# Kernel tuning notes

Hardware: AMD Instinct MI355X
Metric: run time of the kernel (lower is better)

The kernel has to match this reference:

```python
import jax, jax.numpy as jnp
import numpy as np
from jax import lax

B, T, H, C = 1024, 128, 256, 10


def setup_inputs() -> dict:
    key = jax.random.key(0)
    ks = jax.random.split(key, 16)
    inp = {
        "x": jax.random.normal(ks[0], (B, T), dtype=jnp.float32),
        # torch.randn-initialized input weights (input_dim=1)
        "w_gx": jax.random.normal(ks[1], (1, H), dtype=jnp.float32),
        "w_ix": jax.random.normal(ks[2], (1, H), dtype=jnp.float32),
        "w_fx": jax.random.normal(ks[3], (1, H), dtype=jnp.float32),
        "w_ox": jax.random.normal(ks[4], (1, H), dtype=jnp.float32),
        # torch.rand-initialized recurrent weights
        "w_gh": jax.random.uniform(ks[5], (H, H), dtype=jnp.float32),
        "w_ih": jax.random.uniform(ks[6], (H, H), dtype=jnp.float32),
        "w_fh": jax.random.uniform(ks[7], (H, H), dtype=jnp.float32),
        "w_oh": jax.random.uniform(ks[8], (H, H), dtype=jnp.float32),
        "b_g": jax.random.uniform(ks[9], (H,), dtype=jnp.float32),
        "b_i": jax.random.uniform(ks[10], (H,), dtype=jnp.float32),
        "b_f": jax.random.uniform(ks[11], (H,), dtype=jnp.float32),
        "b_o": jax.random.uniform(ks[12], (H,), dtype=jnp.float32),
        "w_ph": jax.random.normal(ks[13], (H, C), dtype=jnp.float32),
        "b_p": jax.random.uniform(ks[14], (C,), dtype=jnp.float32),
    }
    return inp


def reference(x, w_gx, w_ix, w_fx, w_ox, w_gh, w_ih, w_fh, w_oh,
              b_g, b_i, b_f, b_o, w_ph, b_p):
    # Fuse the 4 gate projections into one GEMM per step (same math, order: g,i,f,o)
    Wx = jnp.concatenate([w_gx, w_ix, w_fx, w_ox], axis=1)   # (1, 4H)
    Wh = jnp.concatenate([w_gh, w_ih, w_fh, w_oh], axis=1)   # (H, 4H)
    b = jnp.concatenate([b_g, b_i, b_f, b_o])                 # (4H,)
    h0 = jnp.zeros((x.shape[0], w_gh.shape[0]), dtype=x.dtype)
    c0 = jnp.zeros_like(h0)

    def step(carry, xt):
        h, c = carry
        # xt: (B,) scalar input per example -> (B,1) @ (1,4H)
        z = xt[:, None] @ Wx + h @ Wh + b                     # (B, 4H)
        g, i, f, o = jnp.split(z, 4, axis=1)
        g = jnp.tanh(g)
        i = jax.nn.sigmoid(i)
        f = jax.nn.sigmoid(f)
        o = jax.nn.sigmoid(o)
        c = g * i + c * f
        h = jnp.tanh(c) * o
        return (h, c), None

    (h, _), _ = lax.scan(step, (h0, c0), x.T)                  # scan over time (T, B)
    return h @ w_ph + b_p                                      # (B, num_classes)
```

## Files before the change

kernel.cpp:

```cpp
#include <hip/hip_runtime.h>


#define TSTEPS  128
#define HDIM    256
#define NCLS    10
#define BB      4
#define NBLOCKS 256
#define NTHR    512

#define XSTR    132
#define HSTR    320
#define PSTR    260

typedef char  i8x16 __attribute__((ext_vector_type(16)));
typedef int   i32x4 __attribute__((ext_vector_type(4)));

#define L2E     1.4426950408889634f
#define MGC     (-2.0f * L2E)
#define SMG     (-2.0f * L2E / 16129.0f)
#define SMS     (-1.0f * L2E / 16129.0f)

static __device__ __forceinline__ float rcpf(float x) { return __builtin_amdgcn_rcpf(x); }
static __device__ __forceinline__ float exp2f_fast(float x) { return __builtin_amdgcn_exp2f(x); }

#define MFMA_I8(ACC, A, B) \
    asm("v_mfma_i32_16x16x64_i8 %0, %1, %2, %0" : "+v"(ACC) : "v"(A), "a"(B))

__global__ __launch_bounds__(64)
void pack_w(const float* __restrict__ wg, const float* __restrict__ wi,
            const float* __restrict__ wf, const float* __restrict__ wo,
            signed char* __restrict__ wq8)
{
    const int b = blockIdx.x;
    const int q = b >> 8;
    const int u = b & 255;
    const float* wp = (q == 0) ? wg : (q == 1) ? wi : (q == 2) ? wf : wo;
    const int t  = threadIdx.x;
    const int k0 = t * 4;
    unsigned int pk = 0;
#pragma unroll
    for (int i = 0; i < 4; ++i) {
        const float v = wp[(k0 + i) * HDIM + u];
        int qv = __float2int_rn(v * 127.0f);
        qv = (qv > 127) ? 127 : ((qv < -127) ? -127 : qv);
        pk |= ((unsigned int)qv & 255u) << (8 * i);
    }
    *(unsigned int*)(wq8 + ((size_t)(q * 256 + u) * 256 + k0)) = pk;
}

__global__ __launch_bounds__(NTHR, 2)
void lstm_full(const float* __restrict__ x,
               const float* __restrict__ w_gx, const float* __restrict__ w_ix,
               const float* __restrict__ w_fx, const float* __restrict__ w_ox,
               const float* __restrict__ b_g,  const float* __restrict__ b_i,
               const float* __restrict__ b_f,  const float* __restrict__ b_o,
               const float* __restrict__ w_ph, const float* __restrict__ b_p,
               const signed char* __restrict__ wq8,
               float* __restrict__ out)
{
    const int g    = blockIdx.x;
    const int tid  = threadIdx.x;
    const int w    = tid >> 6;
    const int lane = tid & 63;
    const int l16  = lane & 15;
    const int lq   = lane >> 4;

    __shared__ float        x_lds[BB * XSTR];
    __shared__ signed char  h_q[2][BB * HSTR];
    __shared__ float        proj[BB * PSTR];

    {
        const float* xs = x + (size_t)g * BB * TSTEPS;
        for (int i = tid; i < BB * TSTEPS; i += NTHR)
            x_lds[(i >> 7) * XSTR + (i & 127)] = xs[i];
    }

    i32x4 wa[4][2][4];
#pragma unroll
    for (int q = 0; q < 4; ++q)
#pragma unroll
        for (int ut = 0; ut < 2; ++ut) {
            const int u = w * 32 + ut * 16 + l16;
#pragma unroll
            for (int kk = 0; kk < 4; ++kk) {
                const signed char* p = wq8 + ((size_t)(q * 256 + u) * 256)
                                           + kk * 64 + lq * 16;
                i32x4 v = __builtin_bit_cast(i32x4, *(const i8x16*)p);
                asm volatile("" : "+a"(v));
                wa[q][ut][kk] = v;
            }
        }

    const float* const wxp[4] = {w_gx, w_ix, w_fx, w_ox};
    const float* const bbp[4] = {b_g, b_i, b_f, b_o};
    float wxm[4][2], bm[4][2];
#pragma unroll
    for (int q = 0; q < 4; ++q)
#pragma unroll
        for (int ut = 0; ut < 2; ++ut) {
            const int u = w * 32 + ut * 16 + l16;
            const float m = (q == 0) ? MGC : (-L2E);
            wxm[q][ut] = wxp[q][u] * m;
            bm[q][ut]  = bbp[q][u] * m;
        }

    float c[2] = {0.f, 0.f};
    const bool s0 = (lq & 1) != 0;
    const bool s1 = (lq & 2) != 0;

    __syncthreads();

    for (int t = 0; t < TSTEPS; ++t) {
        i32x4 ah[4];
        if (t > 0) {
            const signed char* hs = &h_q[t & 1][(l16 & 3) * HSTR];
#pragma unroll
            for (int kk = 0; kk < 4; ++kk)
                ah[kk] = *(const i32x4*)(hs + kk * 64 + lq * 16);
        }

        i32x4 a0[4] = {{0,0,0,0},{0,0,0,0},{0,0,0,0},{0,0,0,0}};
        i32x4 a1[4] = {{0,0,0,0},{0,0,0,0},{0,0,0,0},{0,0,0,0}};
        if (t > 0) {
#pragma unroll
            for (int kk = 0; kk < 4; ++kk)
#pragma unroll
                for (int q = 0; q < 4; ++q)
                    MFMA_I8(a0[q], ah[kk], wa[q][0][kk]);
#pragma unroll
            for (int kk = 0; kk < 4; ++kk)
#pragma unroll
                for (int q = 0; q < 4; ++q)
                    MFMA_I8(a1[q], ah[kk], wa[q][1][kk]);
        }

        const float xv = x_lds[lq * XSTR + t];
        signed char* hd = &h_q[(t + 1) & 1][0];
#pragma unroll
        for (int ut = 0; ut < 2; ++ut) {
            float zs[4];
#pragma unroll
            for (int q = 0; q < 4; ++q) {
                const i32x4 v = ut ? a1[q] : a0[q];
                const int lo = s0 ? v[1] : v[0];
                const int hi = s0 ? v[3] : v[2];
                const int av = s1 ? hi : lo;
                const float sm = (q == 0) ? SMG : SMS;
                zs[q] = __builtin_fmaf((float)av, sm,
                        __builtin_fmaf(xv, wxm[q][ut], bm[q][ut]));
            }
            const float gg = 2.0f * rcpf(1.0f + exp2f_fast(zs[0])) - 1.0f;
            const float ii = rcpf(1.0f + exp2f_fast(zs[1]));
            const float ff = rcpf(1.0f + exp2f_fast(zs[2]));
            const float oo = rcpf(1.0f + exp2f_fast(zs[3]));
            const float cc = __builtin_fmaf(c[ut], ff, gg * ii);
            c[ut] = cc;
            const float tc = 2.0f * rcpf(1.0f + exp2f_fast(cc * MGC)) - 1.0f;
            const float hh = tc * oo;
            const int   hq = __float2int_rn(hh * 127.0f);
            const int   u  = w * 32 + ut * 16 + l16;
            hd[lq * HSTR + u] = (signed char)hq;
            if (t == TSTEPS - 1) proj[lq * PSTR + u] = hh;
        }
        __syncthreads();
    }

    if (tid < BB * NCLS) {
        const int r = tid / NCLS, cls = tid - r * NCLS;
        float a = b_p[cls];
#pragma unroll 8
        for (int u = 0; u < HDIM; ++u)
            a = __builtin_fmaf(proj[r * PSTR + u], w_ph[u * NCLS + cls], a);
        out[(size_t)(g * BB + r) * NCLS + cls] = a;
    }
}

extern "C" void kernel_launch(void* const* d_in, const int* in_sizes, int n_in,
                              void* d_out, int out_size, void* d_ws, size_t ws_size,
                              hipStream_t stream)
{
    const float* x    = (const float*)d_in[0];
    const float* w_gx = (const float*)d_in[1];
    const float* w_ix = (const float*)d_in[2];
    const float* w_fx = (const float*)d_in[3];
    const float* w_ox = (const float*)d_in[4];
    const float* w_gh = (const float*)d_in[5];
    const float* w_ih = (const float*)d_in[6];
    const float* w_fh = (const float*)d_in[7];
    const float* w_oh = (const float*)d_in[8];
    const float* b_g  = (const float*)d_in[9];
    const float* b_i  = (const float*)d_in[10];
    const float* b_f  = (const float*)d_in[11];
    const float* b_o  = (const float*)d_in[12];
    const float* w_ph = (const float*)d_in[13];
    const float* b_p  = (const float*)d_in[14];

    signed char* wq8 = (signed char*)d_ws;

    hipLaunchKernelGGL(pack_w, dim3(1024), dim3(64), 0, stream,
                       w_gh, w_ih, w_fh, w_oh, wq8);

    hipLaunchKernelGGL(lstm_full, dim3(NBLOCKS), dim3(NTHR), 0, stream,
                       x, w_gx, w_ix, w_fx, w_ox,
                       b_g, b_i, b_f, b_o, w_ph, b_p,
                       wq8, (float*)d_out);
}
```

Before: 132.2 us.

## Interleave gate math with MFMA chain, peel first step, pack h stores

Peels the t=0 step, which has no recurrent term, out of the loop. The second half-tile's MFMAs are interleaved with the first half-tile's gate transcendentals so MFMA latency can hide VALU work. The K dimension of the packed weights is permuted so each thread writes its two hidden units as one 16-bit LDS store instead of two byte stores. The rest of the recurrence is unchanged, but the weight packing and the h layout now depend on each other.

```diff
diff --git a/kernel.cpp b/kernel.cpp
--- a/kernel.cpp
+++ b/kernel.cpp
@@ -25,6 +25,24 @@
 
 #define MFMA_I8(ACC, A, B) \
     asm("v_mfma_i32_16x16x64_i8 %0, %1, %2, %0" : "+v"(ACC) : "v"(A), "a"(B))
+
+#define EXTRACT(V) (s1 ? (s0 ? (V)[3] : (V)[2]) : (s0 ? (V)[1] : (V)[0]))
+
+static __device__ __forceinline__ float gate_h(float zs0, float zs1, float zs2,
+                                               float zs3, float& c)
+{
+    const float eg = exp2f_fast(zs0), ei = exp2f_fast(zs1);
+    const float ef = exp2f_fast(zs2), eo = exp2f_fast(zs3);
+    const float rg = rcpf(1.0f + eg), ri = rcpf(1.0f + ei);
+    const float rf = rcpf(1.0f + ef), ro = rcpf(1.0f + eo);
+    const float gg = __builtin_fmaf(2.0f, rg, -1.0f);
+    const float cc = __builtin_fmaf(c, rf, gg * ri);
+    c = cc;
+    const float et = exp2f_fast(cc * MGC);
+    const float rt = rcpf(1.0f + et);
+    const float tc = __builtin_fmaf(2.0f, rt, -1.0f);
+    return tc * ro;
+}
 
 __global__ __launch_bounds__(64)
 void pack_w(const float* __restrict__ wg, const float* __restrict__ wi,
@@ -40,7 +58,9 @@
     unsigned int pk = 0;
 #pragma unroll
     for (int i = 0; i < 4; ++i) {
-        const float v = wp[(k0 + i) * HDIM + u];
+        const int k   = k0 + i;
+        const int src = (k & 0xE0) | ((k & 1) << 4) | ((k >> 1) & 15);
+        const float v = wp[src * HDIM + u];
         int qv = __float2int_rn(v * 127.0f);
         qv = (qv > 127) ? 127 : ((qv < -127) ? -127 : qv);
         pk |= ((unsigned int)qv & 255u) << (8 * i);
@@ -104,63 +124,100 @@
             bm[q][ut]  = bbp[q][u] * m;
         }
 
-    float c[2] = {0.f, 0.f};
+    float c0 = 0.f, c1 = 0.f;
     const bool s0 = (lq & 1) != 0;
     const bool s1 = (lq & 2) != 0;
+    const int  woff = lq * HSTR + w * 32 + l16 * 2;
+    const int  u0 = w * 32 + l16, u1 = u0 + 16;
 
     __syncthreads();
 
-    for (int t = 0; t < TSTEPS; ++t) {
-        i32x4 ah[4];
-        if (t > 0) {
-            const signed char* hs = &h_q[t & 1][(l16 & 3) * HSTR];
-#pragma unroll
-            for (int kk = 0; kk < 4; ++kk)
-                ah[kk] = *(const i32x4*)(hs + kk * 64 + lq * 16);
-        }
+    {
+        const float xv = x_lds[lq * XSTR + 0];
+        float zs[2][4];
+#pragma unroll
+        for (int ut = 0; ut < 2; ++ut)
+#pragma unroll
+            for (int q = 0; q < 4; ++q)
+                zs[ut][q] = __builtin_fmaf(xv, wxm[q][ut], bm[q][ut]);
+        const float h0 = gate_h(zs[0][0], zs[0][1], zs[0][2], zs[0][3], c0);
+        const float h1 = gate_h(zs[1][0], zs[1][1], zs[1][2], zs[1][3], c1);
+        const int hq0 = __float2int_rn(h0 * 127.0f);
+        const int hq1 = __float2int_rn(h1 * 127.0f);
+        *(unsigned short*)(&h_q[1][woff]) =
+            (unsigned short)((hq0 & 255) | ((hq1 & 255) << 8));
+        __syncthreads();
+    }
+
+    for (int t = 1; t < TSTEPS; ++t) {
+        const signed char* hs = &h_q[t & 1][(l16 & 3) * HSTR];
+        i32x4 ah0 = *(const i32x4*)(hs +   0 + lq * 16);
+        i32x4 ah1 = *(const i32x4*)(hs +  64 + lq * 16);
+        i32x4 ah2 = *(const i32x4*)(hs + 128 + lq * 16);
+        i32x4 ah3 = *(const i32x4*)(hs + 192 + lq * 16);
 
         i32x4 a0[4] = {{0,0,0,0},{0,0,0,0},{0,0,0,0},{0,0,0,0}};
         i32x4 a1[4] = {{0,0,0,0},{0,0,0,0},{0,0,0,0},{0,0,0,0}};
-        if (t > 0) {
-#pragma unroll
-            for (int kk = 0; kk < 4; ++kk)
-#pragma unroll
-                for (int q = 0; q < 4; ++q)
-                    MFMA_I8(a0[q], ah[kk], wa[q][0][kk]);
-#pragma unroll
-            for (int kk = 0; kk < 4; ++kk)
-#pragma unroll
-                for (int q = 0; q < 4; ++q)
-                    MFMA_I8(a1[q], ah[kk], wa[q][1][kk]);
-        }
+
+#pragma unroll
+        for (int q = 0; q < 4; ++q) MFMA_I8(a0[q], ah0, wa[q][0][0]);
+#pragma unroll
+        for (int q = 0; q < 4; ++q) MFMA_I8(a0[q], ah1, wa[q][0][1]);
+#pragma unroll
+        for (int q = 0; q < 4; ++q) MFMA_I8(a0[q], ah2, wa[q][0][2]);
+#pragma unroll
+        for (int q = 0; q < 4; ++q) MFMA_I8(a0[q], ah3, wa[q][0][3]);
 
         const float xv = x_lds[lq * XSTR + t];
-        signed char* hd = &h_q[(t + 1) & 1][0];
-#pragma unroll
-        for (int ut = 0; ut < 2; ++ut) {
-            float zs[4];
-#pragma unroll
-            for (int q = 0; q < 4; ++q) {
-                const i32x4 v = ut ? a1[q] : a0[q];
-                const int lo = s0 ? v[1] : v[0];
-                const int hi = s0 ? v[3] : v[2];
-                const int av = s1 ? hi : lo;
-                const float sm = (q == 0) ? SMG : SMS;
-                zs[q] = __builtin_fmaf((float)av, sm,
-                        __builtin_fmaf(xv, wxm[q][ut], bm[q][ut]));
-            }
-            const float gg = 2.0f * rcpf(1.0f + exp2f_fast(zs[0])) - 1.0f;
-            const float ii = rcpf(1.0f + exp2f_fast(zs[1]));
-            const float ff = rcpf(1.0f + exp2f_fast(zs[2]));
-            const float oo = rcpf(1.0f + exp2f_fast(zs[3]));
-            const float cc = __builtin_fmaf(c[ut], ff, gg * ii);
-            c[ut] = cc;
-            const float tc = 2.0f * rcpf(1.0f + exp2f_fast(cc * MGC)) - 1.0f;
-            const float hh = tc * oo;
-            const int   hq = __float2int_rn(hh * 127.0f);
-            const int   u  = w * 32 + ut * 16 + l16;
-            hd[lq * HSTR + u] = (signed char)hq;
-            if (t == TSTEPS - 1) proj[lq * PSTR + u] = hh;
+
+#pragma unroll
+        for (int q = 0; q < 4; ++q) MFMA_I8(a1[q], ah0, wa[q][1][0]);
+        float zs00 = __builtin_fmaf((float)EXTRACT(a0[0]), SMG,
+                     __builtin_fmaf(xv, wxm[0][0], bm[0][0]));
+        float zs01 = __builtin_fmaf((float)EXTRACT(a0[1]), SMS,
+                     __builtin_fmaf(xv, wxm[1][0], bm[1][0]));
+#pragma unroll
+        for (int q = 0; q < 4; ++q) MFMA_I8(a1[q], ah1, wa[q][1][1]);
+        float zs02 = __builtin_fmaf((float)EXTRACT(a0[2]), SMS,
+                     __builtin_fmaf(xv, wxm[2][0], bm[2][0]));
+        float zs03 = __builtin_fmaf((float)EXTRACT(a0[3]), SMS,
+                     __builtin_fmaf(xv, wxm[3][0], bm[3][0]));
+#pragma unroll
+        for (int q = 0; q < 4; ++q) MFMA_I8(a1[q], ah2, wa[q][1][2]);
+        const float eg0 = exp2f_fast(zs00), ei0 = exp2f_fast(zs01);
+        const float ef0 = exp2f_fast(zs02), eo0 = exp2f_fast(zs03);
+        const float sg0 = 1.0f + eg0, si0 = 1.0f + ei0;
+        const float sf0 = 1.0f + ef0, so0 = 1.0f + eo0;
+#pragma unroll
+        for (int q = 0; q < 4; ++q) MFMA_I8(a1[q], ah3, wa[q][1][3]);
+        const float rg0 = rcpf(sg0), ri0 = rcpf(si0);
+        const float rf0 = rcpf(sf0), ro0 = rcpf(so0);
+        const float gg0 = __builtin_fmaf(2.0f, rg0, -1.0f);
+        const float cc0 = __builtin_fmaf(c0, rf0, gg0 * ri0);
+        c0 = cc0;
+
+        const float et0 = exp2f_fast(cc0 * MGC);
+        float zs10 = __builtin_fmaf((float)EXTRACT(a1[0]), SMG,
+                     __builtin_fmaf(xv, wxm[0][1], bm[0][1]));
+        float zs11 = __builtin_fmaf((float)EXTRACT(a1[1]), SMS,
+                     __builtin_fmaf(xv, wxm[1][1], bm[1][1]));
+        float zs12 = __builtin_fmaf((float)EXTRACT(a1[2]), SMS,
+                     __builtin_fmaf(xv, wxm[2][1], bm[2][1]));
+        float zs13 = __builtin_fmaf((float)EXTRACT(a1[3]), SMS,
+                     __builtin_fmaf(xv, wxm[3][1], bm[3][1]));
+        const float rt0 = rcpf(1.0f + et0);
+        const float tc0 = __builtin_fmaf(2.0f, rt0, -1.0f);
+        const float hh0 = tc0 * ro0;
+        const float hh1 = gate_h(zs10, zs11, zs12, zs13, c1);
+
+        const int hq0 = __float2int_rn(hh0 * 127.0f);
+        const int hq1 = __float2int_rn(hh1 * 127.0f);
+        *(unsigned short*)(&h_q[(t + 1) & 1][woff]) =
+            (unsigned short)((hq0 & 255) | ((hq1 & 255) << 8));
+
+        if (t == TSTEPS - 1) {
+            proj[lq * PSTR + u0] = hh0;
+            proj[lq * PSTR + u1] = hh1;
         }
         __syncthreads();
     }
```

New measurement: 135.3 us. 1.02x slower.

## Double waves per block so each wave handles one 16-unit hidden tile

Applied to the files above, without the earlier changes.

Raises the block to 1024 threads (16 waves), so each wave owns 16 hidden units instead of 32. This halves the per-wave MFMA chain and gate math per timestep and shortens the serial critical path between barriers. It also peels step 0, which has no recurrent term, out of the loop to drop the per-step branches. The trade-off is a more expensive barrier across 16 waves and the need for 4 blocks of 1024 threads to fit per CU, which leaves fewer registers per thread.

```diff
diff --git a/kernel.cpp b/kernel.cpp
--- a/kernel.cpp
+++ b/kernel.cpp
@@ -6,7 +6,7 @@
 #define NCLS    10
 #define BB      4
 #define NBLOCKS 256
-#define NTHR    512
+#define NTHR    1024
 
 #define XSTR    132
 #define HSTR    320
@@ -25,6 +25,24 @@
 
 #define MFMA_I8(ACC, A, B) \
     asm("v_mfma_i32_16x16x64_i8 %0, %1, %2, %0" : "+v"(ACC) : "v"(A), "a"(B))
+
+#define EXTRACT(V) (s1 ? (s0 ? (V)[3] : (V)[2]) : (s0 ? (V)[1] : (V)[0]))
+
+static __device__ __forceinline__ float gate_h(float zs0, float zs1, float zs2,
+                                               float zs3, float& c)
+{
+    const float eg = exp2f_fast(zs0), ei = exp2f_fast(zs1);
+    const float ef = exp2f_fast(zs2), eo = exp2f_fast(zs3);
+    const float rg = rcpf(1.0f + eg), ri = rcpf(1.0f + ei);
+    const float rf = rcpf(1.0f + ef), ro = rcpf(1.0f + eo);
+    const float gg = __builtin_fmaf(2.0f, rg, -1.0f);
+    const float cc = __builtin_fmaf(c, rf, gg * ri);
+    c = cc;
+    const float et = exp2f_fast(cc * MGC);
+    const float rt = rcpf(1.0f + et);
+    const float tc = __builtin_fmaf(2.0f, rt, -1.0f);
+    return tc * ro;
+}
 
 __global__ __launch_bounds__(64)
 void pack_w(const float* __restrict__ wg, const float* __restrict__ wi,
@@ -48,7 +66,7 @@
     *(unsigned int*)(wq8 + ((size_t)(q * 256 + u) * 256 + k0)) = pk;
 }
 
-__global__ __launch_bounds__(NTHR, 2)
+__global__ __launch_bounds__(NTHR, 4)
 void lstm_full(const float* __restrict__ x,
                const float* __restrict__ w_gx, const float* __restrict__ w_ix,
                const float* __restrict__ w_fx, const float* __restrict__ w_ox,
@@ -75,93 +93,76 @@
             x_lds[(i >> 7) * XSTR + (i & 127)] = xs[i];
     }
 
-    i32x4 wa[4][2][4];
+    const int u = w * 16 + l16;
+    i32x4 wa[4][4];
 #pragma unroll
     for (int q = 0; q < 4; ++q)
 #pragma unroll
-        for (int ut = 0; ut < 2; ++ut) {
-            const int u = w * 32 + ut * 16 + l16;
-#pragma unroll
-            for (int kk = 0; kk < 4; ++kk) {
-                const signed char* p = wq8 + ((size_t)(q * 256 + u) * 256)
-                                           + kk * 64 + lq * 16;
-                i32x4 v = __builtin_bit_cast(i32x4, *(const i8x16*)p);
-                asm volatile("" : "+a"(v));
-                wa[q][ut][kk] = v;
-            }
+        for (int kk = 0; kk < 4; ++kk) {
+            const signed char* p = wq8 + ((size_t)(q * 256 + u) * 256)
+                                       + kk * 64 + lq * 16;
+            i32x4 v = __builtin_bit_cast(i32x4, *(const i8x16*)p);
+            asm volatile("" : "+a"(v));
+            wa[q][kk] = v;
         }
 
     const float* const wxp[4] = {w_gx, w_ix, w_fx, w_ox};
     const float* const bbp[4] = {b_g, b_i, b_f, b_o};
-    float wxm[4][2], bm[4][2];
-#pragma unroll
-    for (int q = 0; q < 4; ++q)
-#pragma unroll
-        for (int ut = 0; ut < 2; ++ut) {
-            const int u = w * 32 + ut * 16 + l16;
-            const float m = (q == 0) ? MGC : (-L2E);
-            wxm[q][ut] = wxp[q][u] * m;
-            bm[q][ut]  = bbp[q][u] * m;
-        }
-
-    float c[2] = {0.f, 0.f};
+    float wxm[4], bm[4];
+#pragma unroll
+    for (int q = 0; q < 4; ++q) {
+        const float m = (q == 0) ? MGC : (-L2E);
+        wxm[q] = wxp[q][u] * m;
+        bm[q]  = bbp[q][u] * m;
+    }
+
+    float c = 0.f;
     const bool s0 = (lq & 1) != 0;
     const bool s1 = (lq & 2) != 0;
+    const int  woff = lq * HSTR + u;
 
     __syncthreads();
 
-    for (int t = 0; t < TSTEPS; ++t) {
-        i32x4 ah[4];
-        if (t > 0) {
-            const signed char* hs = &h_q[t & 1][(l16 & 3) * HSTR];
-#pragma unroll
-            for (int kk = 0; kk < 4; ++kk)
-                ah[kk] = *(const i32x4*)(hs + kk * 64 + lq * 16);
-        }
-
-        i32x4 a0[4] = {{0,0,0,0},{0,0,0,0},{0,0,0,0},{0,0,0,0}};
-        i32x4 a1[4] = {{0,0,0,0},{0,0,0,0},{0,0,0,0},{0,0,0,0}};
-        if (t > 0) {
-#pragma unroll
-            for (int kk = 0; kk < 4; ++kk)
-#pragma unroll
-                for (int q = 0; q < 4; ++q)
-                    MFMA_I8(a0[q], ah[kk], wa[q][0][kk]);
-#pragma unroll
-            for (int kk = 0; kk < 4; ++kk)
-#pragma unroll
-                for (int q = 0; q < 4; ++q)
-                    MFMA_I8(a1[q], ah[kk], wa[q][1][kk]);
-        }
+    {
+        const float xv = x_lds[lq * XSTR + 0];
+        const float hh = gate_h(__builtin_fmaf(xv, wxm[0], bm[0]),
+                                __builtin_fmaf(xv, wxm[1], bm[1]),
+                                __builtin_fmaf(xv, wxm[2], bm[2]),
+                                __builtin_fmaf(xv, wxm[3], bm[3]), c);
+        h_q[1][woff] = (signed char)__float2int_rn(hh * 127.0f);
+        __syncthreads();
+    }
+
+    for (int t = 1; t < TSTEPS; ++t) {
+        const signed char* hs = &h_q[t & 1][(l16 & 3) * HSTR];
+        const i32x4 ah0 = *(const i32x4*)(hs +   0 + lq * 16);
+        const i32x4 ah1 = *(const i32x4*)(hs +  64 + lq * 16);
+        const i32x4 ah2 = *(const i32x4*)(hs + 128 + lq * 16);
+        const i32x4 ah3 = *(const i32x4*)(hs + 192 + lq * 16);
+
+        i32x4 a[4] = {{0,0,0,0},{0,0,0,0},{0,0,0,0},{0,0,0,0}};
+#pragma unroll
+        for (int q = 0; q < 4; ++q) MFMA_I8(a[q], ah0, wa[q][0]);
+#pragma unroll
+        for (int q = 0; q < 4; ++q) MFMA_I8(a[q], ah1, wa[q][1]);
+#pragma unroll
+        for (int q = 0; q < 4; ++q) MFMA_I8(a[q], ah2, wa[q][2]);
+#pragma unroll
+        for (int q = 0; q < 4; ++q) MFMA_I8(a[q], ah3, wa[q][3]);
 
         const float xv = x_lds[lq * XSTR + t];
-        signed char* hd = &h_q[(t + 1) & 1][0];
-#pragma unroll
-        for (int ut = 0; ut < 2; ++ut) {
-            float zs[4];
-#pragma unroll
-            for (int q = 0; q < 4; ++q) {
-                const i32x4 v = ut ? a1[q] : a0[q];
-                const int lo = s0 ? v[1] : v[0];
-                const int hi = s0 ? v[3] : v[2];
-                const int av = s1 ? hi : lo;
-                const float sm = (q == 0) ? SMG : SMS;
-                zs[q] = __builtin_fmaf((float)av, sm,
-                        __builtin_fmaf(xv, wxm[q][ut], bm[q][ut]));
-            }
-            const float gg = 2.0f * rcpf(1.0f + exp2f_fast(zs[0])) - 1.0f;
-            const float ii = rcpf(1.0f + exp2f_fast(zs[1]));
-            const float ff = rcpf(1.0f + exp2f_fast(zs[2]));
-            const float oo = rcpf(1.0f + exp2f_fast(zs[3]));
-            const float cc = __builtin_fmaf(c[ut], ff, gg * ii);
-            c[ut] = cc;
-            const float tc = 2.0f * rcpf(1.0f + exp2f_fast(cc * MGC)) - 1.0f;
-            const float hh = tc * oo;
-            const int   hq = __float2int_rn(hh * 127.0f);
-            const int   u  = w * 32 + ut * 16 + l16;
-            hd[lq * HSTR + u] = (signed char)hq;
-            if (t == TSTEPS - 1) proj[lq * PSTR + u] = hh;
-        }
+        const float zs0 = __builtin_fmaf((float)EXTRACT(a[0]), SMG,
+                          __builtin_fmaf(xv, wxm[0], bm[0]));
+        const float zs1 = __builtin_fmaf((float)EXTRACT(a[1]), SMS,
+                          __builtin_fmaf(xv, wxm[1], bm[1]));
+        const float zs2 = __builtin_fmaf((float)EXTRACT(a[2]), SMS,
+                          __builtin_fmaf(xv, wxm[2], bm[2]));
+        const float zs3 = __builtin_fmaf((float)EXTRACT(a[3]), SMS,
+                          __builtin_fmaf(xv, wxm[3], bm[3]));
+        const float hh = gate_h(zs0, zs1, zs2, zs3, c);
+
+        h_q[(t + 1) & 1][woff] = (signed char)__float2int_rn(hh * 127.0f);
+        if (t == TSTEPS - 1) proj[lq * PSTR + u] = hh;
         __syncthreads();
     }
 
@@ -169,8 +170,8 @@
         const int r = tid / NCLS, cls = tid - r * NCLS;
         float a = b_p[cls];
 #pragma unroll 8
-        for (int u = 0; u < HDIM; ++u)
-            a = __builtin_fmaf(proj[r * PSTR + u], w_ph[u * NCLS + cls], a);
+        for (int uu = 0; uu < HDIM; ++uu)
+            a = __builtin_fmaf(proj[r * PSTR + uu], w_ph[uu * NCLS + cls], a);
         out[(size_t)(g * BB + r) * NCLS + cls] = a;
     }
 }
```

Result: faster. 124.6 us (median of 2 runs) (-5.8%).
